# Performance work log

Measured on AMD Instinct MI355X. Metric: run time of the kernel, lower is better.

## Reference

```python
import jax, jax.numpy as jnp
import numpy as np

NUM_HEADS = 16
HEAD_DIM = 128  # hidden_size 2048 / 16 heads


def setup_inputs() -> dict:
    key = jax.random.key(0)
    k1, k2, k3 = jax.random.split(key, 3)
    bsz, seq, hidden = 2, 2048, 2048
    return {
        "query": jax.random.normal(k1, (bsz, seq, hidden), dtype=jnp.float32),
        "key": jax.random.normal(k2, (bsz, seq, hidden), dtype=jnp.float32),
        "value": jax.random.normal(k3, (bsz, seq, hidden), dtype=jnp.float32),
        "attention_mask": jnp.zeros((1, 1, seq, seq), dtype=jnp.float32),
    }


def reference(query, key, value, attention_mask):
    bsz, seq, hidden = query.shape
    h, d = NUM_HEADS, HEAD_DIM
    # (b, s, h*d) -> (b, h, s, d)
    q = query.reshape(bsz, seq, h, d).transpose(0, 2, 1, 3)
    k = key.reshape(bsz, seq, h, d).transpose(0, 2, 1, 3)
    v = value.reshape(bsz, seq, h, d).transpose(0, 2, 1, 3)
    # scores: (b, h, s, s)
    scores = jnp.einsum("bhqd,bhkd->bhqk", q, k) / jnp.sqrt(jnp.float32(d))
    scores = scores + attention_mask
    probs = jax.nn.softmax(scores.astype(jnp.float32), axis=-1).astype(q.dtype)
    out = jnp.einsum("bhqk,bhkd->bhqd", probs, v)
    # (b, h, s, d) -> (b, s, h*d)
    return out.transpose(0, 2, 1, 3).reshape(bsz, seq, hidden)
```

## Files before the change

kernel.cpp:

```cpp
#include <hip/hip_runtime.h>
#include <hip/hip_bf16.h>
#include <math.h>

#define SEQ 2048
#define NH 16
#define HD 128
#define HID 2048
#define KVB 64
#define NKT (SEQ/KVB)
#define QB 128
#define QBLK 64

typedef __attribute__((ext_vector_type(8))) short bf16x8;
typedef __attribute__((ext_vector_type(4))) short bf16x4;
typedef __attribute__((ext_vector_type(4))) float f32x4;
typedef __attribute__((ext_vector_type(16))) float f32x16;
typedef __attribute__((ext_vector_type(2))) unsigned uint2v;

#define SCL2E 0.1275310261f
#define L2E   1.4426950408889634f

__device__ __forceinline__ short f2bf(float x){
  __hip_bfloat16 h = __float2bfloat16(x);
  return *reinterpret_cast<short*>(&h);
}

__device__ __forceinline__ unsigned cvtpk(float lo, float hi){
  unsigned r;
  asm("v_cvt_pk_bf16_f32 %0, %1, %2" : "=v"(r) : "v"(lo), "v"(hi));
  return r;
}

__device__ __forceinline__ void gld_lds16(const void* g, void* l){
  __builtin_amdgcn_global_load_lds((const __attribute__((address_space(1))) void*)g,
                                   (__attribute__((address_space(3))) void*)l, 16, 0, 0);
}

__global__ void mask_scan_k(const float* __restrict__ m, int n4, int* __restrict__ flag){
  int any = 0;
  const float4* m4 = (const float4*)m;
  for (int i = blockIdx.x*blockDim.x + threadIdx.x; i < n4; i += gridDim.x*blockDim.x){
    float4 v = m4[i];
    any |= (v.x != 0.f) | (v.y != 0.f) | (v.z != 0.f) | (v.w != 0.f);
  }
  if (__ballot(any) != 0ull && (threadIdx.x & 63) == 0) atomicOr(flag, 1);
}

__global__ void cvt_qk_k(const float* __restrict__ in, short* __restrict__ out){
  const int n4 = (2*SEQ*HID)/4;
  for (int i = blockIdx.x*blockDim.x + threadIdx.x; i < n4; i += gridDim.x*blockDim.x){
    int i4 = i*4;
    int b   = i4 >> 22;
    int rem = i4 & ((1<<22)-1);
    int s   = rem >> 11;
    int hd  = rem & 2047;
    int h = hd >> 7, d = hd & 127;
    float4 v = *(const float4*)(in + i4);
    bf16x4 o; o[0]=f2bf(v.x); o[1]=f2bf(v.y); o[2]=f2bf(v.z); o[3]=f2bf(v.w);
    *(bf16x4*)(out + ((size_t)((b*NH + h)*SEQ + s))*HD + d) = o;
  }
}

__global__ void cvt_vt_k(const float* __restrict__ Vg, short* __restrict__ Vt){
  __shared__ short T[64*HD];
  const int bh = blockIdx.x >> 5, st = blockIdx.x & 31;
  const int b = bh >> 4, h = bh & 15;
  const int s0 = st*64;
  const int tid = threadIdx.x;
  const float* vp = Vg + ((size_t)(b*SEQ + s0))*HID + h*HD;
  #pragma unroll
  for (int i = 0; i < 8; ++i){
    int idx = tid + i*256;
    int r = idx >> 5, c4 = idx & 31;
    float4 v = *(const float4*)(vp + (size_t)r*HID + c4*4);
    int X = ((r & 7) ^ ((r >> 3) & 7)) << 3;
    bf16x4 o; o[0]=f2bf(v.x); o[1]=f2bf(v.y); o[2]=f2bf(v.z); o[3]=f2bf(v.w);
    *(bf16x4*)(&T[r*HD + ((c4*4) ^ X)]) = o;
  }
  __syncthreads();
  short* op = Vt + ((size_t)bh*HD)*SEQ + s0;
  #pragma unroll
  for (int u = 0; u < 4; ++u){
    int unit = tid + u*256;
    int sb = unit & 7, d = unit >> 3;
    bf16x8 pk;
    #pragma unroll
    for (int j = 0; j < 8; ++j)
      pk[j] = T[(sb*8 + j)*HD + (d ^ (((j ^ sb) & 7) << 3))];
    *(bf16x8*)(op + (size_t)d*SEQ + sb*8) = pk;
  }
}

__launch_bounds__(256, 2)
__global__ void attn_p5_k(const float* __restrict__ Qg, const short* __restrict__ Kbp,
                          const short* __restrict__ Vtb, const float* __restrict__ Mg,
                          float* __restrict__ Og, const int* __restrict__ flagp)
{
  __shared__ __align__(16) short Kl[2][KVB*HD];
  __shared__ __align__(16) short Vl[2][HD*KVB];

  const int tid = threadIdx.x;
  const int w = tid >> 6, lane = tid & 63;
  const int l31 = lane & 31, hi1 = lane >> 5;
  const int swz = (lane & 7) << 3;

  int bid = blockIdx.x;
  bid = (bid & 7)*64 + (bid >> 3);
  const int bh = bid >> 4;
  const int qt = bid & 15;
  const int b = bh >> 4, h = bh & 15;
  const int mflag = *flagp;
  const int qrow_g = qt*QB + w*32 + l31;

  bf16x8 qf[8];
  {
    const float* qrow = Qg + ((size_t)(b*SEQ + qrow_g))*HID + h*HD;
    #pragma unroll
    for (int ks = 0; ks < 8; ++ks){
      float4 a = *(const float4*)(qrow + ks*16 + hi1*8);
      float4 c = *(const float4*)(qrow + ks*16 + hi1*8 + 4);
      bf16x8 q;
      q[0]=f2bf(a.x*SCL2E); q[1]=f2bf(a.y*SCL2E); q[2]=f2bf(a.z*SCL2E); q[3]=f2bf(a.w*SCL2E);
      q[4]=f2bf(c.x*SCL2E); q[5]=f2bf(c.y*SCL2E); q[6]=f2bf(c.z*SCL2E); q[7]=f2bf(c.w*SCL2E);
      qf[ks] = q;
    }
  }

  const short* kbase = Kbp + (size_t)bh*SEQ*HD;
  const short* vbase = Vtb + (size_t)bh*HD*SEQ;
  int koff[4], voff[4], cdst[4];
  #pragma unroll
  for (int c = 0; c < 4; ++c){
    int p = (c*4 + w)*1024 + lane*16;
    cdst[c] = (c*4 + w)*1024;
    int r  = p >> 8;
    int cs = (p & 255) >> 1;
    koff[c] = r*HD + (cs ^ ((r & 7) << 3));
    int d   = p >> 7;
    int cs2 = (p & 127) >> 1;
    voff[c] = d*SEQ + (cs2 ^ ((d & 7) << 3));
  }
  auto stageK = [&](int kt){
    const short* ks = kbase + kt*(KVB*HD);
    char* kl = (char*)&Kl[kt & 1][0];
    #pragma unroll
    for (int c = 0; c < 4; ++c) gld_lds16(ks + koff[c], kl + cdst[c]);
  };
  auto stageV = [&](int kt){
    const short* vs = vbase + kt*KVB;
    char* vl = (char*)&Vl[kt & 1][0];
    #pragma unroll
    for (int c = 0; c < 4; ++c) gld_lds16(vs + voff[c], vl + cdst[c]);
  };

  f32x16 acc[4];
  #pragma unroll
  for (int cb = 0; cb < 4; ++cb)
    #pragma unroll
    for (int i = 0; i < 16; ++i) acc[cb][i] = 0.f;
  float m_ = -INFINITY, l_ = 0.f;

  auto qkt = [&](int kt, f32x16& s0, f32x16& s1){
    const short* Kc = &Kl[kt & 1][0];
    f32x16 a0, a1;
    #pragma unroll
    for (int i = 0; i < 16; ++i){ a0[i] = 0.f; a1[i] = 0.f; }
    __builtin_amdgcn_s_setprio(1);
    #pragma unroll
    for (int ks = 0; ks < 8; ++ks){
      int o = (ks*16 + hi1*8) ^ swz;
      bf16x8 kf0 = *(const bf16x8*)(Kc + l31*HD + o);
      bf16x8 kf1 = *(const bf16x8*)(Kc + (32 + l31)*HD + o);
      a0 = __builtin_amdgcn_mfma_f32_32x32x16_bf16(kf0, qf[ks], a0, 0, 0, 0);
      a1 = __builtin_amdgcn_mfma_f32_32x32x16_bf16(kf1, qf[ks], a1, 0, 0, 0);
    }
    __builtin_amdgcn_s_setprio(0);
    s0 = a0; s1 = a1;
  };

  stageK(0); stageV(0); stageK(1);
  asm volatile("s_waitcnt vmcnt(8)" ::: "memory");
  __builtin_amdgcn_s_barrier();
  f32x16 svE0, svE1, svO0, svO1;
  qkt(0, svE0, svE1);

#define SUBSTEP(T, C0, C1, N0, N1, DOSV, DOSK, VMC, DOQ, DOBAR) do {              \
    if (DOSV) stageV((T)+1);                                                      \
    if (DOSK) stageK((T)+2);                                                      \
    float p[32];                                                                  \
    if (mflag){                                                                   \
      const float* mrow = Mg + (size_t)qrow_g*SEQ + (T)*KVB;                      \
      _Pragma("unroll")                                                           \
      for (int i = 0; i < 16; ++i){                                               \
        int kv0 = (i&3) + 8*(i>>2) + 4*hi1;                                       \
        p[i]    = C0[i] + mrow[kv0]*L2E;                                          \
        p[16+i] = C1[i] + mrow[32+kv0]*L2E;                                       \
      }                                                                           \
    } else {                                                                      \
      _Pragma("unroll")                                                           \
      for (int i = 0; i < 16; ++i){ p[i] = C0[i]; p[16+i] = C1[i]; }              \
    }                                                                             \
    asm volatile("s_waitcnt vmcnt(" VMC ")" ::: "memory");                        \
    __builtin_amdgcn_s_barrier();                                                 \
    if (DOQ) qkt((T)+1, N0, N1);                                                  \
    float pm;                                                                     \
    {                                                                             \
      float t16[16];                                                              \
      _Pragma("unroll")                                                           \
      for (int i = 0; i < 16; ++i) t16[i] = fmaxf(p[i], p[i+16]);                 \
      float t8[8];                                                                \
      _Pragma("unroll")                                                           \
      for (int i = 0; i < 8; ++i) t8[i] = fmaxf(t16[i], t16[i+8]);                \
      float t4[4];                                                                \
      _Pragma("unroll")                                                           \
      for (int i = 0; i < 4; ++i) t4[i] = fmaxf(t8[i], t8[i+4]);                  \
      pm = fmaxf(fmaxf(t4[0], t4[1]), fmaxf(t4[2], t4[3]));                       \
      uint2v rr = __builtin_amdgcn_permlane32_swap(__float_as_uint(pm), __float_as_uint(pm), false, false); \
      pm = fmaxf(__uint_as_float(rr[0]), __uint_as_float(rr[1]));                 \
    }                                                                             \
    float mn = fmaxf(m_, pm);                                                     \
    if (!__all(pm - m_ <= 8.0f)){                                                 \
      float fac = exp2f(m_ - mn);                                                 \
      m_ = mn; l_ *= fac;                                                         \
      _Pragma("unroll")                                                           \
      for (int cb = 0; cb < 4; ++cb)                                              \
        _Pragma("unroll")                                                         \
        for (int i = 0; i < 16; ++i) acc[cb][i] *= fac;                           \
    }                                                                             \
    {                                                                             \
      float s16[16];                                                              \
      _Pragma("unroll")                                                           \
      for (int i = 0; i < 16; ++i){                                               \
        float e0 = exp2f(p[i] - m_);                                              \
        float e1 = exp2f(p[i+16] - m_);                                           \
        p[i] = e0; p[i+16] = e1;                                                  \
        s16[i] = e0 + e1;                                                         \
      }                                                                           \
      float s8[8];                                                                \
      _Pragma("unroll")                                                           \
      for (int i = 0; i < 8; ++i) s8[i] = s16[i] + s16[i+8];                      \
      float s4[4];                                                                \
      _Pragma("unroll")                                                           \
      for (int i = 0; i < 4; ++i) s4[i] = s8[i] + s8[i+4];                        \
      float rs = (s4[0] + s4[1]) + (s4[2] + s4[3]);                               \
      uint2v rr = __builtin_amdgcn_permlane32_swap(__float_as_uint(rs), __float_as_uint(rs), false, false); \
      rs = __uint_as_float(rr[0]) + __uint_as_float(rr[1]);                       \
      l_ += rs;                                                                   \
    }                                                                             \
    bf16x8 pa[4];                                                                 \
    _Pragma("unroll")                                                             \
    for (int sl = 0; sl < 4; ++sl){                                               \
      const int ib = 8*(sl & 1) + 16*(sl >> 1);                                   \
      unsigned A0 = cvtpk(p[ib+0], p[ib+1]);                                      \
      unsigned A1 = cvtpk(p[ib+2], p[ib+3]);                                      \
      unsigned B0 = cvtpk(p[ib+4], p[ib+5]);                                      \
      unsigned B1 = cvtpk(p[ib+6], p[ib+7]);                                      \
      uint2v r0 = __builtin_amdgcn_permlane32_swap(A0, B0, false, false);         \
      uint2v r1 = __builtin_amdgcn_permlane32_swap(A1, B1, false, false);         \
      union { unsigned u[4]; bf16x8 v; } tt;                                      \
      tt.u[0] = r0[0]; tt.u[1] = r1[0]; tt.u[2] = r0[1]; tt.u[3] = r1[1];         \
      pa[sl] = tt.v;                                                              \
    }                                                                             \
    {                                                                             \
      const short* Vc = &Vl[(T) & 1][0];                                          \
      __builtin_amdgcn_s_setprio(1);                                              \
      _Pragma("unroll")                                                           \
      for (int sl = 0; sl < 4; ++sl){                                             \
        int o = (sl*16 + hi1*8) ^ swz;                                            \
        _Pragma("unroll")                                                         \
        for (int cb = 0; cb < 4; ++cb){                                           \
          bf16x8 vf = *(const bf16x8*)(Vc + (cb*32 + l31)*KVB + o);               \
          acc[cb] = __builtin_amdgcn_mfma_f32_32x32x16_bf16(vf, pa[sl], acc[cb], 0, 0, 0); \
        }                                                                         \
      }                                                                           \
      __builtin_amdgcn_s_setprio(0);                                              \
    }                                                                             \
    if (DOBAR) __builtin_amdgcn_s_barrier();                                      \
  } while(0)

  for (int t = 0; t < NKT-2; t += 2){
    SUBSTEP(t,   svE0, svE1, svO0, svO1, 1, 1, "8", 1, 1);
    SUBSTEP(t+1, svO0, svO1, svE0, svE1, 1, 1, "8", 1, 1);
  }
  SUBSTEP(NKT-2, svE0, svE1, svO0, svO1, 1, 0, "4", 1, 1);
  SUBSTEP(NKT-1, svO0, svO1, svE0, svE1, 0, 0, "0", 0, 0);
#undef SUBSTEP

  float inv = 1.0f / l_;
  float* orow = Og + ((size_t)(b*SEQ + qrow_g))*HID + h*HD;
  #pragma unroll
  for (int cb = 0; cb < 4; ++cb)
    #pragma unroll
    for (int g = 0; g < 4; ++g){
      float4 o;
      o.x = acc[cb][g*4+0]*inv; o.y = acc[cb][g*4+1]*inv;
      o.z = acc[cb][g*4+2]*inv; o.w = acc[cb][g*4+3]*inv;
      *(float4*)(orow + cb*32 + g*8 + 4*hi1) = o;
    }
}

__launch_bounds__(256)
__global__ void attn_f32_k(const float* __restrict__ Qg, const float* __restrict__ Kg,
                           const float* __restrict__ Vg, const float* __restrict__ Mg,
                           float* __restrict__ Og, const int* __restrict__ flagp)
{
  __shared__ __align__(16) short Kl[KVB*HD];
  __shared__ __align__(16) short Vt[HD*KVB];
  __shared__ __align__(16) short Pl[4][16*KVB];

  const int tid  = threadIdx.x;
  const int w    = tid >> 6;
  const int lane = tid & 63;
  const int lo   = lane & 15;
  const int hi   = lane >> 4;

  int bid = blockIdx.x;
  bid = (bid & 7)*128 + (bid >> 3);
  const int bh = bid >> 5;
  const int qt = bid & 31;
  const int b  = bh >> 4;
  const int h  = bh & 15;
  const int mflag = *flagp;

  bf16x8 qf[4];
  {
    const float* qrow = Qg + ((size_t)(b*SEQ + qt*QBLK + w*16 + lo))*HID + h*HD;
    #pragma unroll
    for (int kc = 0; kc < 4; ++kc){
      float4 v0 = *(const float4*)(qrow + kc*32 + hi*8);
      float4 v1 = *(const float4*)(qrow + kc*32 + hi*8 + 4);
      bf16x8 q;
      q[0]=f2bf(v0.x); q[1]=f2bf(v0.y); q[2]=f2bf(v0.z); q[3]=f2bf(v0.w);
      q[4]=f2bf(v1.x); q[5]=f2bf(v1.y); q[6]=f2bf(v1.z); q[7]=f2bf(v1.w);
      qf[kc] = q;
    }
  }

  f32x4 acc[8];
  #pragma unroll
  for (int i = 0; i < 8; ++i){ acc[i][0]=0.f; acc[i][1]=0.f; acc[i][2]=0.f; acc[i][3]=0.f; }
  float mrow[4] = {-INFINITY, -INFINITY, -INFINITY, -INFINITY};
  float lrow[4] = {0.f, 0.f, 0.f, 0.f};

  const float* kb = Kg + ((size_t)b*SEQ)*HID + h*HD;
  const float* vb = Vg + ((size_t)b*SEQ)*HID + h*HD;

  for (int kt = 0; kt < NKT; ++kt){
    __syncthreads();
    {
      const float* kp = kb + (size_t)(kt*KVB)*HID;
      #pragma unroll
      for (int i = 0; i < 8; ++i){
        int idx = tid + i*256;
        int r  = idx >> 5;
        int c4 = idx & 31;
        float4 v = *(const float4*)(kp + (size_t)r*HID + c4*4);
        int sidx = (r*HD + c4*4) ^ ((r & 7) << 3);
        short* dst = &Kl[sidx];
        dst[0]=f2bf(v.x); dst[1]=f2bf(v.y); dst[2]=f2bf(v.z); dst[3]=f2bf(v.w);
      }
      const float* vp = vb + (size_t)(kt*KVB)*HID;
      #pragma unroll
      for (int u = 0; u < 4; ++u){
        int unit = tid + u*256;
        int d   = unit & 127;
        int g   = unit >> 7;
        int kv0 = g*8;
        bf16x8 pk;
        #pragma unroll
        for (int j = 0; j < 8; ++j)
          pk[j] = f2bf(vp[(size_t)(kv0 + j)*HID + d]);
        int sidx = (d*KVB + kv0) ^ ((d & 7) << 3);
        *(bf16x8*)(&Vt[sidx]) = pk;
      }
    }
    __syncthreads();

    f32x4 sv[4];
    #pragma unroll
    for (int nb = 0; nb < 4; ++nb){ sv[nb][0]=0.f; sv[nb][1]=0.f; sv[nb][2]=0.f; sv[nb][3]=0.f; }
    #pragma unroll
    for (int nb = 0; nb < 4; ++nb){
      int krow = nb*16 + lo;
      #pragma unroll
      for (int kc = 0; kc < 4; ++kc){
        int sidx = (krow*HD + kc*32 + hi*8) ^ ((krow & 7) << 3);
        bf16x8 kf = *(const bf16x8*)(&Kl[sidx]);
        sv[nb] = __builtin_amdgcn_mfma_f32_16x16x32_bf16(qf[kc], kf, sv[nb], 0, 0, 0);
      }
    }

    float p[4][4];
    if (mflag){
      #pragma unroll
      for (int nb = 0; nb < 4; ++nb)
        #pragma unroll
        for (int r = 0; r < 4; ++r){
          float mv = Mg[(size_t)(qt*QBLK + w*16 + hi*4 + r)*SEQ + kt*KVB + nb*16 + lo];
          p[nb][r] = sv[nb][r]*SCL2E + mv*L2E;
        }
    } else {
      #pragma unroll
      for (int nb = 0; nb < 4; ++nb)
        #pragma unroll
        for (int r = 0; r < 4; ++r)
          p[nb][r] = sv[nb][r]*SCL2E;
    }

    #pragma unroll
    for (int r = 0; r < 4; ++r){
      float mx = fmaxf(fmaxf(p[0][r], p[1][r]), fmaxf(p[2][r], p[3][r]));
      mx = fmaxf(mx, __shfl_xor(mx, 1, 64));
      mx = fmaxf(mx, __shfl_xor(mx, 2, 64));
      mx = fmaxf(mx, __shfl_xor(mx, 4, 64));
      mx = fmaxf(mx, __shfl_xor(mx, 8, 64));
      float mn  = fmaxf(mrow[r], mx);
      float fac = exp2f(mrow[r] - mn);
      mrow[r] = mn;
      lrow[r] *= fac;
      #pragma unroll
      for (int oc = 0; oc < 8; ++oc) acc[oc][r] *= fac;
      float rsv = 0.f;
      #pragma unroll
      for (int nb = 0; nb < 4; ++nb){
        float e = exp2f(p[nb][r] - mn);
        p[nb][r] = e;
        rsv += e;
      }
      rsv += __shfl_xor(rsv, 1, 64);
      rsv += __shfl_xor(rsv, 2, 64);
      rsv += __shfl_xor(rsv, 4, 64);
      rsv += __shfl_xor(rsv, 8, 64);
      lrow[r] += rsv;
    }

    short* myP = &Pl[w][0];
    #pragma unroll
    for (int nb = 0; nb < 4; ++nb)
      #pragma unroll
      for (int r = 0; r < 4; ++r){
        int row = hi*4 + r;
        int sidx = (row*KVB + nb*16 + lo) ^ ((row & 7) << 3);
        myP[sidx] = f2bf(p[nb][r]);
      }

    #pragma unroll
    for (int kc2 = 0; kc2 < 2; ++kc2){
      int sA = (lo*KVB + kc2*32 + hi*8) ^ ((lo & 7) << 3);
      bf16x8 pa = *(const bf16x8*)(&myP[sA]);
      #pragma unroll
      for (int oc = 0; oc < 8; ++oc){
        int vrow = oc*16 + lo;
        int sB = (vrow*KVB + kc2*32 + hi*8) ^ ((vrow & 7) << 3);
        bf16x8 vf = *(const bf16x8*)(&Vt[sB]);
        acc[oc] = __builtin_amdgcn_mfma_f32_16x16x32_bf16(pa, vf, acc[oc], 0, 0, 0);
      }
    }
  }

  float* orow = Og + ((size_t)(b*SEQ + qt*QBLK + w*16))*HID + h*HD;
  #pragma unroll
  for (int r = 0; r < 4; ++r){
    float inv = 1.0f / lrow[r];
    #pragma unroll
    for (int oc = 0; oc < 8; ++oc)
      orow[(size_t)(hi*4 + r)*HID + oc*16 + lo] = acc[oc][r]*inv;
  }
}

extern "C" void kernel_launch(void* const* d_in, const int* in_sizes, int n_in,
                              void* d_out, int out_size, void* d_ws, size_t ws_size,
                              hipStream_t stream)
{
  const float* Qg = (const float*)d_in[0];
  const float* Kg = (const float*)d_in[1];
  const float* Vg = (const float*)d_in[2];
  const float* Mg = (const float*)d_in[3];
  float* Og = (float*)d_out;
  int* flag = (int*)d_ws;

  const size_t plane = (size_t)2*NH*SEQ*HD;
  const size_t need = 64 + 2*plane*sizeof(short);

  hipMemsetAsync(d_ws, 0, 4, stream);
  hipLaunchKernelGGL(mask_scan_k, dim3(256), dim3(256), 0, stream, Mg, SEQ*SEQ/4, flag);

  if (ws_size >= need){
    short* Kb = (short*)((char*)d_ws + 64);
    short* Vt = Kb + plane;
    hipLaunchKernelGGL(cvt_qk_k, dim3(2048), dim3(256), 0, stream, Kg, Kb);
    hipLaunchKernelGGL(cvt_vt_k, dim3(1024), dim3(256), 0, stream, Vg, Vt);
    hipLaunchKernelGGL(attn_p5_k, dim3(512), dim3(256), 0, stream, Qg, Kb, Vt, Mg, Og, flag);
  } else {
    hipLaunchKernelGGL(attn_f32_k, dim3(32*32), dim3(256), 0, stream, Qg, Kg, Vg, Mg, Og, flag);
  }
}
```

Before: 132.2 us.

## Use 8-wave 256-row Q tiles with 4-stage KV LDS pipeline

The attention kernel now uses 512 threads (8 waves) per block, each block covering 256 query rows, so each K/V tile loaded into LDS is shared by twice as many waves. The grid shrinks to 256 blocks. K and V staging is merged into one stage function with a 4-deep ring buffer prefetching three tiles ahead, and the prefetch starts before the Q load. LDS use doubles to 128KB per block, and with only 256 blocks occupancy and load balance across CUs may suffer.

```diff
diff --git a/kernel.cpp b/kernel.cpp
--- a/kernel.cpp
+++ b/kernel.cpp
@@ -8,7 +8,7 @@
 #define HID 2048
 #define KVB 64
 #define NKT (SEQ/KVB)
-#define QB 128
+#define QB 256
 #define QBLK 64
 
 typedef __attribute__((ext_vector_type(8))) short bf16x8;
@@ -91,13 +91,13 @@
   }
 }
 
-__launch_bounds__(256, 2)
-__global__ void attn_p5_k(const float* __restrict__ Qg, const short* __restrict__ Kbp,
+__launch_bounds__(512, 2)
+__global__ void attn_w8_k(const float* __restrict__ Qg, const short* __restrict__ Kbp,
                           const short* __restrict__ Vtb, const float* __restrict__ Mg,
                           float* __restrict__ Og, const int* __restrict__ flagp)
 {
-  __shared__ __align__(16) short Kl[2][KVB*HD];
-  __shared__ __align__(16) short Vl[2][HD*KVB];
+  __shared__ __align__(16) short Kl[4][KVB*HD];
+  __shared__ __align__(16) short Vl[4][HD*KVB];
 
   const int tid = threadIdx.x;
   const int w = tid >> 6, lane = tid & 63;
@@ -105,12 +105,40 @@
   const int swz = (lane & 7) << 3;
 
   int bid = blockIdx.x;
-  bid = (bid & 7)*64 + (bid >> 3);
-  const int bh = bid >> 4;
-  const int qt = bid & 15;
+  bid = (bid & 7)*32 + (bid >> 3);
+  const int bh = bid >> 3;
+  const int qt = bid & 7;
   const int b = bh >> 4, h = bh & 15;
   const int mflag = *flagp;
   const int qrow_g = qt*QB + w*32 + l31;
+
+  const short* kbase = Kbp + (size_t)bh*SEQ*HD;
+  const short* vbase = Vtb + (size_t)bh*HD*SEQ;
+  int koff[2], voff[2], cdst[2];
+  #pragma unroll
+  for (int c = 0; c < 2; ++c){
+    int p = c*8192 + w*1024 + lane*16;
+    cdst[c] = c*8192 + w*1024;
+    int r  = p >> 8;
+    int cs = (p & 255) >> 1;
+    koff[c] = r*HD + (cs ^ ((r & 7) << 3));
+    int d   = p >> 7;
+    int cs2 = (p & 127) >> 1;
+    voff[c] = d*SEQ + (cs2 ^ ((d & 7) << 3));
+  }
+  auto stage = [&](int kt){
+    const short* ks = kbase + kt*(KVB*HD);
+    const short* vs = vbase + kt*KVB;
+    char* kl = (char*)&Kl[kt & 3][0];
+    char* vl = (char*)&Vl[kt & 3][0];
+    #pragma unroll
+    for (int c = 0; c < 2; ++c){
+      gld_lds16(ks + koff[c], kl + cdst[c]);
+      gld_lds16(vs + voff[c], vl + cdst[c]);
+    }
+  };
+
+  stage(0); stage(1); stage(2);
 
   bf16x8 qf[8];
   {
@@ -126,33 +154,6 @@
     }
   }
 
-  const short* kbase = Kbp + (size_t)bh*SEQ*HD;
-  const short* vbase = Vtb + (size_t)bh*HD*SEQ;
-  int koff[4], voff[4], cdst[4];
-  #pragma unroll
-  for (int c = 0; c < 4; ++c){
-    int p = (c*4 + w)*1024 + lane*16;
-    cdst[c] = (c*4 + w)*1024;
-    int r  = p >> 8;
-    int cs = (p & 255) >> 1;
-    koff[c] = r*HD + (cs ^ ((r & 7) << 3));
-    int d   = p >> 7;
-    int cs2 = (p & 127) >> 1;
-    voff[c] = d*SEQ + (cs2 ^ ((d & 7) << 3));
-  }
-  auto stageK = [&](int kt){
-    const short* ks = kbase + kt*(KVB*HD);
-    char* kl = (char*)&Kl[kt & 1][0];
-    #pragma unroll
-    for (int c = 0; c < 4; ++c) gld_lds16(ks + koff[c], kl + cdst[c]);
-  };
-  auto stageV = [&](int kt){
-    const short* vs = vbase + kt*KVB;
-    char* vl = (char*)&Vl[kt & 1][0];
-    #pragma unroll
-    for (int c = 0; c < 4; ++c) gld_lds16(vs + voff[c], vl + cdst[c]);
-  };
-
   f32x16 acc[4];
   #pragma unroll
   for (int cb = 0; cb < 4; ++cb)
@@ -161,7 +162,7 @@
   float m_ = -INFINITY, l_ = 0.f;
 
   auto qkt = [&](int kt, f32x16& s0, f32x16& s1){
-    const short* Kc = &Kl[kt & 1][0];
+    const short* Kc = &Kl[kt & 3][0];
     f32x16 a0, a1;
     #pragma unroll
     for (int i = 0; i < 16; ++i){ a0[i] = 0.f; a1[i] = 0.f; }
@@ -178,15 +179,13 @@
     s0 = a0; s1 = a1;
   };
 
-  stageK(0); stageV(0); stageK(1);
   asm volatile("s_waitcnt vmcnt(8)" ::: "memory");
   __builtin_amdgcn_s_barrier();
   f32x16 svE0, svE1, svO0, svO1;
   qkt(0, svE0, svE1);
 
-#define SUBSTEP(T, C0, C1, N0, N1, DOSV, DOSK, VMC, DOQ, DOBAR) do {              \
-    if (DOSV) stageV((T)+1);                                                      \
-    if (DOSK) stageK((T)+2);                                                      \
+#define SUBSTEP(T, C0, C1, N0, N1, DOST, VMC, DOQ, DOBAR) do {                    \
+    if (DOST) stage((T)+3);                                                       \
     float p[32];                                                                  \
     if (mflag){                                                                   \
       const float* mrow = Mg + (size_t)qrow_g*SEQ + (T)*KVB;                      \
@@ -262,7 +261,7 @@
       pa[sl] = tt.v;                                                              \
     }                                                                             \
     {                                                                             \
-      const short* Vc = &Vl[(T) & 1][0];                                          \
+      const short* Vc = &Vl[(T) & 3][0];                                          \
       __builtin_amdgcn_s_setprio(1);                                              \
       _Pragma("unroll")                                                           \
       for (int sl = 0; sl < 4; ++sl){                                             \
@@ -278,12 +277,14 @@
     if (DOBAR) __builtin_amdgcn_s_barrier();                                      \
   } while(0)
 
-  for (int t = 0; t < NKT-2; t += 2){
-    SUBSTEP(t,   svE0, svE1, svO0, svO1, 1, 1, "8", 1, 1);
-    SUBSTEP(t+1, svO0, svO1, svE0, svE1, 1, 1, "8", 1, 1);
-  }
-  SUBSTEP(NKT-2, svE0, svE1, svO0, svO1, 1, 0, "4", 1, 1);
-  SUBSTEP(NKT-1, svO0, svO1, svE0, svE1, 0, 0, "0", 0, 0);
+  for (int t = 0; t < NKT-4; t += 2){
+    SUBSTEP(t,   svE0, svE1, svO0, svO1, 1, "8", 1, 1);
+    SUBSTEP(t+1, svO0, svO1, svE0, svE1, 1, "8", 1, 1);
+  }
+  SUBSTEP(NKT-4, svE0, svE1, svO0, svO1, 1, "8", 1, 1);
+  SUBSTEP(NKT-3, svO0, svO1, svE0, svE1, 0, "4", 1, 1);
+  SUBSTEP(NKT-2, svE0, svE1, svO0, svO1, 0, "0", 1, 1);
+  SUBSTEP(NKT-1, svO0, svO1, svE0, svE1, 0, "0", 0, 0);
 #undef SUBSTEP
 
   float inv = 1.0f / l_;
@@ -490,7 +491,7 @@
     short* Vt = Kb + plane;
     hipLaunchKernelGGL(cvt_qk_k, dim3(2048), dim3(256), 0, stream, Kg, Kb);
     hipLaunchKernelGGL(cvt_vt_k, dim3(1024), dim3(256), 0, stream, Vg, Vt);
-    hipLaunchKernelGGL(attn_p5_k, dim3(512), dim3(256), 0, stream, Qg, Kb, Vt, Mg, Og, flag);
+    hipLaunchKernelGGL(attn_w8_k, dim3(256), dim3(512), 0, stream, Qg, Kb, Vt, Mg, Og, flag);
   } else {
     hipLaunchKernelGGL(attn_f32_k, dim3(32*32), dim3(256), 0, stream, Qg, Kg, Vg, Mg, Og, flag);
   }
```

New measurement: 134.1 us. No clear change (+1.4%).

## Merge K/V conversion kernels, widen K LDS swizzle, drop setprio, add sched barriers

Applied to the files above, without the earlier changes.

Combines the K bf16 conversion and V transpose-conversion into one launch with a block-index split, removing one kernel launch and its tail. The K tile LDS swizzle is widened from 8 to 16 row phases, and the read offset is adjusted to match, to reduce bank conflicts in the 32x32 MFMA K-fragment reads. The s_setprio hints around the MFMA loops are removed, and barriers are wrapped in sched_barrier fences so the compiler cannot move code across them. The fallback kernel only has its KVB constants spelled out as 64.

```diff
diff --git a/kernel.cpp b/kernel.cpp
--- a/kernel.cpp
+++ b/kernel.cpp
@@ -24,16 +24,21 @@
   __hip_bfloat16 h = __float2bfloat16(x);
   return *reinterpret_cast<short*>(&h);
 }
-
 __device__ __forceinline__ unsigned cvtpk(float lo, float hi){
   unsigned r;
   asm("v_cvt_pk_bf16_f32 %0, %1, %2" : "=v"(r) : "v"(lo), "v"(hi));
   return r;
 }
-
 __device__ __forceinline__ void gld_lds16(const void* g, void* l){
   __builtin_amdgcn_global_load_lds((const __attribute__((address_space(1))) void*)g,
                                    (__attribute__((address_space(3))) void*)l, 16, 0, 0);
+}
+__device__ __forceinline__ void block_barrier(){
+  asm volatile("" ::: "memory");
+  __builtin_amdgcn_sched_barrier(0);
+  __builtin_amdgcn_s_barrier();
+  __builtin_amdgcn_sched_barrier(0);
+  asm volatile("" ::: "memory");
 }
 
 __global__ void mask_scan_k(const float* __restrict__ m, int n4, int* __restrict__ flag){
@@ -46,55 +51,57 @@
   if (__ballot(any) != 0ull && (threadIdx.x & 63) == 0) atomicOr(flag, 1);
 }
 
-__global__ void cvt_qk_k(const float* __restrict__ in, short* __restrict__ out){
-  const int n4 = (2*SEQ*HID)/4;
-  for (int i = blockIdx.x*blockDim.x + threadIdx.x; i < n4; i += gridDim.x*blockDim.x){
-    int i4 = i*4;
-    int b   = i4 >> 22;
-    int rem = i4 & ((1<<22)-1);
-    int s   = rem >> 11;
-    int hd  = rem & 2047;
-    int h = hd >> 7, d = hd & 127;
-    float4 v = *(const float4*)(in + i4);
-    bf16x4 o; o[0]=f2bf(v.x); o[1]=f2bf(v.y); o[2]=f2bf(v.z); o[3]=f2bf(v.w);
-    *(bf16x4*)(out + ((size_t)((b*NH + h)*SEQ + s))*HD + d) = o;
-  }
-}
-
-__global__ void cvt_vt_k(const float* __restrict__ Vg, short* __restrict__ Vt){
+__global__ void cvt_kv_k(const float* __restrict__ Kg, const float* __restrict__ Vg,
+                         short* __restrict__ Kb, short* __restrict__ Vt){
   __shared__ short T[64*HD];
-  const int bh = blockIdx.x >> 5, st = blockIdx.x & 31;
-  const int b = bh >> 4, h = bh & 15;
-  const int s0 = st*64;
   const int tid = threadIdx.x;
-  const float* vp = Vg + ((size_t)(b*SEQ + s0))*HID + h*HD;
-  #pragma unroll
-  for (int i = 0; i < 8; ++i){
-    int idx = tid + i*256;
-    int r = idx >> 5, c4 = idx & 31;
-    float4 v = *(const float4*)(vp + (size_t)r*HID + c4*4);
-    int X = ((r & 7) ^ ((r >> 3) & 7)) << 3;
-    bf16x4 o; o[0]=f2bf(v.x); o[1]=f2bf(v.y); o[2]=f2bf(v.z); o[3]=f2bf(v.w);
-    *(bf16x4*)(&T[r*HD + ((c4*4) ^ X)]) = o;
-  }
-  __syncthreads();
-  short* op = Vt + ((size_t)bh*HD)*SEQ + s0;
-  #pragma unroll
-  for (int u = 0; u < 4; ++u){
-    int unit = tid + u*256;
-    int sb = unit & 7, d = unit >> 3;
-    bf16x8 pk;
-    #pragma unroll
-    for (int j = 0; j < 8; ++j)
-      pk[j] = T[(sb*8 + j)*HD + (d ^ (((j ^ sb) & 7) << 3))];
-    *(bf16x8*)(op + (size_t)d*SEQ + sb*8) = pk;
+  if (blockIdx.x < 2048){
+    const int n4 = (2*SEQ*HID)/4;
+    for (int i = blockIdx.x*256 + tid; i < n4; i += 2048*256){
+      int i4 = i*4;
+      int b   = i4 >> 22;
+      int rem = i4 & ((1<<22)-1);
+      int s   = rem >> 11;
+      int hd  = rem & 2047;
+      int h = hd >> 7, d = hd & 127;
+      float4 v = *(const float4*)(Kg + i4);
+      bf16x4 o; o[0]=f2bf(v.x); o[1]=f2bf(v.y); o[2]=f2bf(v.z); o[3]=f2bf(v.w);
+      *(bf16x4*)(Kb + ((size_t)((b*NH + h)*SEQ + s))*HD + d) = o;
+    }
+  } else {
+    const int bid = blockIdx.x - 2048;
+    const int bh = bid >> 5, st = bid & 31;
+    const int b = bh >> 4, h = bh & 15;
+    const int s0 = st*64;
+    const float* vp = Vg + ((size_t)(b*SEQ + s0))*HID + h*HD;
+    #pragma unroll
+    for (int i = 0; i < 8; ++i){
+      int idx = tid + i*256;
+      int r = idx >> 5, c4 = idx & 31;
+      float4 v = *(const float4*)(vp + (size_t)r*HID + c4*4);
+      int X = ((r & 7) ^ ((r >> 3) & 7)) << 3;
+      bf16x4 o; o[0]=f2bf(v.x); o[1]=f2bf(v.y); o[2]=f2bf(v.z); o[3]=f2bf(v.w);
+      *(bf16x4*)(&T[r*HD + ((c4*4) ^ X)]) = o;
+    }
+    __syncthreads();
+    short* op = Vt + ((size_t)bh*HD)*SEQ + s0;
+    #pragma unroll
+    for (int u = 0; u < 4; ++u){
+      int unit = tid + u*256;
+      int sb = unit & 7, d = unit >> 3;
+      bf16x8 pk;
+      #pragma unroll
+      for (int j = 0; j < 8; ++j)
+        pk[j] = T[(sb*8 + j)*HD + (d ^ (((j ^ sb) & 7) << 3))];
+      *(bf16x8*)(op + (size_t)d*SEQ + sb*8) = pk;
+    }
   }
 }
 
 __launch_bounds__(256, 2)
-__global__ void attn_p5_k(const float* __restrict__ Qg, const short* __restrict__ Kbp,
-                          const short* __restrict__ Vtb, const float* __restrict__ Mg,
-                          float* __restrict__ Og, const int* __restrict__ flagp)
+__global__ void attn_p10_k(const float* __restrict__ Qg, const short* __restrict__ Kbp,
+                           const short* __restrict__ Vtb, const float* __restrict__ Mg,
+                           float* __restrict__ Og, const int* __restrict__ flagp)
 {
   __shared__ __align__(16) short Kl[2][KVB*HD];
   __shared__ __align__(16) short Vl[2][HD*KVB];
@@ -102,7 +109,8 @@
   const int tid = threadIdx.x;
   const int w = tid >> 6, lane = tid & 63;
   const int l31 = lane & 31, hi1 = lane >> 5;
-  const int swz = (lane & 7) << 3;
+  const int swzk = (l31 & 15) << 3;
+  const int swzv = (l31 & 7) << 3;
 
   int bid = blockIdx.x;
   bid = (bid & 7)*64 + (bid >> 3);
@@ -135,7 +143,7 @@
     cdst[c] = (c*4 + w)*1024;
     int r  = p >> 8;
     int cs = (p & 255) >> 1;
-    koff[c] = r*HD + (cs ^ ((r & 7) << 3));
+    koff[c] = r*HD + (cs ^ ((r & 15) << 3));
     int d   = p >> 7;
     int cs2 = (p & 127) >> 1;
     voff[c] = d*SEQ + (cs2 ^ ((d & 7) << 3));
@@ -165,22 +173,20 @@
     f32x16 a0, a1;
     #pragma unroll
     for (int i = 0; i < 16; ++i){ a0[i] = 0.f; a1[i] = 0.f; }
-    __builtin_amdgcn_s_setprio(1);
     #pragma unroll
     for (int ks = 0; ks < 8; ++ks){
-      int o = (ks*16 + hi1*8) ^ swz;
+      int o = (ks*16 + hi1*8) ^ swzk;
       bf16x8 kf0 = *(const bf16x8*)(Kc + l31*HD + o);
       bf16x8 kf1 = *(const bf16x8*)(Kc + (32 + l31)*HD + o);
       a0 = __builtin_amdgcn_mfma_f32_32x32x16_bf16(kf0, qf[ks], a0, 0, 0, 0);
       a1 = __builtin_amdgcn_mfma_f32_32x32x16_bf16(kf1, qf[ks], a1, 0, 0, 0);
     }
-    __builtin_amdgcn_s_setprio(0);
     s0 = a0; s1 = a1;
   };
 
   stageK(0); stageV(0); stageK(1);
   asm volatile("s_waitcnt vmcnt(8)" ::: "memory");
-  __builtin_amdgcn_s_barrier();
+  block_barrier();
   f32x16 svE0, svE1, svO0, svO1;
   qkt(0, svE0, svE1);
 
@@ -201,7 +207,7 @@
       for (int i = 0; i < 16; ++i){ p[i] = C0[i]; p[16+i] = C1[i]; }              \
     }                                                                             \
     asm volatile("s_waitcnt vmcnt(" VMC ")" ::: "memory");                        \
-    __builtin_amdgcn_s_barrier();                                                 \
+    block_barrier();                                                              \
     if (DOQ) qkt((T)+1, N0, N1);                                                  \
     float pm;                                                                     \
     {                                                                             \
@@ -263,19 +269,17 @@
     }                                                                             \
     {                                                                             \
       const short* Vc = &Vl[(T) & 1][0];                                          \
-      __builtin_amdgcn_s_setprio(1);                                              \
       _Pragma("unroll")                                                           \
       for (int sl = 0; sl < 4; ++sl){                                             \
-        int o = (sl*16 + hi1*8) ^ swz;                                            \
+        int o = (sl*16 + hi1*8) ^ swzv;                                           \
         _Pragma("unroll")                                                         \
         for (int cb = 0; cb < 4; ++cb){                                           \
           bf16x8 vf = *(const bf16x8*)(Vc + (cb*32 + l31)*KVB + o);               \
           acc[cb] = __builtin_amdgcn_mfma_f32_32x32x16_bf16(vf, pa[sl], acc[cb], 0, 0, 0); \
         }                                                                         \
       }                                                                           \
-      __builtin_amdgcn_s_setprio(0);                                              \
     }                                                                             \
-    if (DOBAR) __builtin_amdgcn_s_barrier();                                      \
+    if (DOBAR) block_barrier();                                                   \
   } while(0)
 
   for (int t = 0; t < NKT-2; t += 2){
@@ -304,9 +308,9 @@
                            const float* __restrict__ Vg, const float* __restrict__ Mg,
                            float* __restrict__ Og, const int* __restrict__ flagp)
 {
-  __shared__ __align__(16) short Kl[KVB*HD];
-  __shared__ __align__(16) short Vt[HD*KVB];
-  __shared__ __align__(16) short Pl[4][16*KVB];
+  __shared__ __align__(16) short Kl[64*HD];
+  __shared__ __align__(16) short Vt[HD*64];
+  __shared__ __align__(16) short Pl[4][16*64];
 
   const int tid  = threadIdx.x;
   const int w    = tid >> 6;
@@ -345,10 +349,10 @@
   const float* kb = Kg + ((size_t)b*SEQ)*HID + h*HD;
   const float* vb = Vg + ((size_t)b*SEQ)*HID + h*HD;
 
-  for (int kt = 0; kt < NKT; ++kt){
+  for (int kt = 0; kt < SEQ/64; ++kt){
     __syncthreads();
     {
-      const float* kp = kb + (size_t)(kt*KVB)*HID;
+      const float* kp = kb + (size_t)(kt*64)*HID;
       #pragma unroll
       for (int i = 0; i < 8; ++i){
         int idx = tid + i*256;
@@ -359,7 +363,7 @@
         short* dst = &Kl[sidx];
         dst[0]=f2bf(v.x); dst[1]=f2bf(v.y); dst[2]=f2bf(v.z); dst[3]=f2bf(v.w);
       }
-      const float* vp = vb + (size_t)(kt*KVB)*HID;
+      const float* vp = vb + (size_t)(kt*64)*HID;
       #pragma unroll
       for (int u = 0; u < 4; ++u){
         int unit = tid + u*256;
@@ -370,7 +374,7 @@
         #pragma unroll
         for (int j = 0; j < 8; ++j)
           pk[j] = f2bf(vp[(size_t)(kv0 + j)*HID + d]);
-        int sidx = (d*KVB + kv0) ^ ((d & 7) << 3);
+        int sidx = (d*64 + kv0) ^ ((d & 7) << 3);
         *(bf16x8*)(&Vt[sidx]) = pk;
       }
     }
@@ -396,7 +400,7 @@
       for (int nb = 0; nb < 4; ++nb)
         #pragma unroll
         for (int r = 0; r < 4; ++r){
-          float mv = Mg[(size_t)(qt*QBLK + w*16 + hi*4 + r)*SEQ + kt*KVB + nb*16 + lo];
+          float mv = Mg[(size_t)(qt*QBLK + w*16 + hi*4 + r)*SEQ + kt*64 + nb*16 + lo];
           p[nb][r] = sv[nb][r]*SCL2E + mv*L2E;
         }
     } else {
@@ -440,18 +444,18 @@
       #pragma unroll
       for (int r = 0; r < 4; ++r){
         int row = hi*4 + r;
-        int sidx = (row*KVB + nb*16 + lo) ^ ((row & 7) << 3);
+        int sidx = (row*64 + nb*16 + lo) ^ ((row & 7) << 3);
         myP[sidx] = f2bf(p[nb][r]);
       }
 
     #pragma unroll
     for (int kc2 = 0; kc2 < 2; ++kc2){
-      int sA = (lo*KVB + kc2*32 + hi*8) ^ ((lo & 7) << 3);
+      int sA = (lo*64 + kc2*32 + hi*8) ^ ((lo & 7) << 3);
       bf16x8 pa = *(const bf16x8*)(&myP[sA]);
       #pragma unroll
       for (int oc = 0; oc < 8; ++oc){
         int vrow = oc*16 + lo;
-        int sB = (vrow*KVB + kc2*32 + hi*8) ^ ((vrow & 7) << 3);
+        int sB = (vrow*64 + kc2*32 + hi*8) ^ ((vrow & 7) << 3);
         bf16x8 vf = *(const bf16x8*)(&Vt[sB]);
         acc[oc] = __builtin_amdgcn_mfma_f32_16x16x32_bf16(pa, vf, acc[oc], 0, 0, 0);
       }
@@ -488,9 +492,8 @@
   if (ws_size >= need){
     short* Kb = (short*)((char*)d_ws + 64);
     short* Vt = Kb + plane;
-    hipLaunchKernelGGL(cvt_qk_k, dim3(2048), dim3(256), 0, stream, Kg, Kb);
-    hipLaunchKernelGGL(cvt_vt_k, dim3(1024), dim3(256), 0, stream, Vg, Vt);
-    hipLaunchKernelGGL(attn_p5_k, dim3(512), dim3(256), 0, stream, Qg, Kb, Vt, Mg, Og, flag);
+    hipLaunchKernelGGL(cvt_kv_k, dim3(3072), dim3(256), 0, stream, Kg, Vg, Kb, Vt);
+    hipLaunchKernelGGL(attn_p10_k, dim3(512), dim3(256), 0, stream, Qg, Kb, Vt, Mg, Og, flag);
   } else {
     hipLaunchKernelGGL(attn_f32_k, dim3(32*32), dim3(256), 0, stream, Qg, Kg, Vg, Mg, Og, flag);
   }
```

After: 128.9 us. -2.5%, faster.
